# Optimization experiments

Measured on AMD Instinct MI355X. Metric: run time of the kernel, lower is better.

Reference implementation:

```python
import jax, jax.numpy as jnp
import numpy as np

DECAY = 0.99
EPS = 1e-05
N_EMBED = 4096

def setup_inputs() -> dict:
    key = jax.random.key(0)
    k1, k2 = jax.random.split(key)
    x = jax.random.normal(k1, (32, 1024, 256), dtype=jnp.float32)
    embed = jax.random.normal(k2, (256, N_EMBED), dtype=jnp.float32)
    cluster_size = jnp.zeros((N_EMBED,), dtype=jnp.float32)
    embed_avg = embed  # buffer initialized as embed.clone()
    return {"x": x, "embed": embed, "cluster_size": cluster_size, "embed_avg": embed_avg}

def reference(x, embed, cluster_size, embed_avg):
    # x: [B, L, D]; embed/embed_avg: [D, K]; cluster_size: [K]
    B, L, D = x.shape
    K = embed.shape[1]
    flat = x.reshape(B * L, D)
    dist = (jnp.sum(flat * flat, axis=1, keepdims=True)
            - 2.0 * flat @ embed
            + jnp.sum(embed * embed, axis=0, keepdims=True))
    embed_indices = jnp.argmin(dist, axis=1)  # [N]
    # one-hot scatter-sum (counts per code)
    embed_onehot_sum = jnp.zeros((K,), dtype=x.dtype).at[embed_indices].add(1.0)
    # EMA updates, faithful to the torch source including its quirks:
    #   cluster_size.mul_(decay).add_(onehot_sum, alpha=1-eps)  (note: 1-eps, not 1-decay)
    #   embed_avg.mul_(decay).add(embed_sum, ...)  -> .add (not in-place), so embed_sum is discarded
    cluster_size_new = cluster_size * DECAY + embed_onehot_sum * (1.0 - EPS)
    embed_avg_new = embed_avg * DECAY
    n = jnp.sum(cluster_size_new)
    cs = (cluster_size_new + EPS) / (n + K * EPS) * n  # Laplace-smoothed counts
    embed_new = embed_avg_new / cs[None, :]  # [D, K], copied into self.embed before lookup
    # codebook lookup with the UPDATED embed (matches embed.data.copy_ ordering)
    quantize = embed_new.T[embed_indices].reshape(B, L, D)
    diff = jnp.mean(jnp.square(jax.lax.stop_gradient(quantize) - x))
    quantize_st = x + jax.lax.stop_gradient(quantize - x)  # straight-through
    return (quantize_st, embed_indices.reshape(B, L), diff,
            cluster_size_new, embed_avg_new, embed_new)
```

## Files before the change

kernel.cpp:

```cpp
#include <hip/hip_runtime.h>
#include <math.h>

constexpr float DECAY = 0.99f;
constexpr float EPS_F = 1e-5f;
constexpr float MARGIN = 0.08f;

typedef short bf16x8 __attribute__((ext_vector_type(8)));
typedef float f32x4 __attribute__((ext_vector_type(4)));
typedef float vf4 __attribute__((ext_vector_type(4)));

#define BM 256
#define KSPLIT 2
#define NU 128
#define NBUF 6
#define D_FIX 256

__device__ __forceinline__ unsigned rne_bf16(float f) {
  unsigned u = __float_as_uint(f);
  return (u + 0x7fffu + ((u >> 16) & 1u)) >> 16;
}
__device__ __forceinline__ unsigned pack_hilo(float v) {
  unsigned u = __float_as_uint(v);
  unsigned hi = u & 0xffff0000u;
  float rem = v - __uint_as_float(hi);
  return hi | rne_bf16(rem);
}

__global__ void k_prepack_enorm(const float* __restrict__ e, ushort* __restrict__ phl,
                                double* __restrict__ e2d, float* __restrict__ e2f, int K) {
  __shared__ ushort tile[8192];
  __shared__ double red[4][64];
  const int ct = blockIdx.x;
  const int t = threadIdx.x;
  for (int du = 0; du < 4; ++du) {
    __syncthreads();
#pragma unroll
    for (int p = 0; p < 16; ++p) {
      int idx = t + p * 256;
      int dl = idx >> 6, col = idx & 63;
      float v = e[(size_t)(du * 64 + dl) * K + ct * 64 + col];
      unsigned pk = pack_hilo(v);
      int pos = col * 64 + (((dl >> 3) ^ (col & 7)) << 3) + (dl & 7);
      tile[pos] = (ushort)(pk >> 16);
      tile[4096 + pos] = (ushort)(pk & 0xffffu);
    }
    __syncthreads();
    uint4* dst = (uint4*)(phl + (size_t)(ct * 4 + du) * 8192);
    const uint4* srcT = (const uint4*)tile;
#pragma unroll
    for (int p = 0; p < 4; ++p) dst[t + p * 256] = srcT[t + p * 256];
  }
  const int kl = t & 63;
  const int part = t >> 6;
  const int k = ct * 64 + kl;
  double s = 0.0;
  for (int d = part; d < D_FIX; d += 4) {
    double v = (double)e[(size_t)d * K + k];
    s = fma(v, v, s);
  }
  red[part][kl] = s;
  __syncthreads();
  if (part == 0) {
    double tt = ((red[0][kl] + red[1][kl]) + red[2][kl]) + red[3][kl];
    e2d[k] = tt;
    e2f[k] = (float)tt;
  }
}

__launch_bounds__(512, 2)
__global__ void k_argmin_mfma(const float* __restrict__ x, const ushort* __restrict__ phl,
                              const float* __restrict__ e2f,
                              float* __restrict__ bestv, float* __restrict__ secv,
                              int* __restrict__ besti, int N, int K) {
  __shared__ ushort es[NBUF][8192];
  __shared__ float e2s[2048];

  const int tid = threadIdx.x;
  const int l   = tid & 63;
  const int w   = tid >> 6;
  const int g   = l >> 4;
  const int c16 = l & 15;

  const int bflat = blockIdx.x + gridDim.x * blockIdx.y;
  const int xcd   = bflat & 7;
  const int slot  = bflat >> 3;
  const int ytile = xcd >> 2;
  const int xtile = (xcd & 3) * (gridDim.x >> 2) + slot;

  const int kbase = ytile * (K / KSPLIT);
  const int rowW  = xtile * BM + w * 32;

  char* esb = (char*)es;
  const size_t unit0 = (size_t)ytile * NU;

  auto stage = [&](int u) {
    const char* gs = (const char*)phl + ((unit0 + (size_t)u) << 14) + (w << 11) + (l << 4);
    char* ld = esb + ((u % NBUF) << 14) + (w << 11) + (l << 4);
    __builtin_amdgcn_global_load_lds((const unsigned*)gs,          (unsigned*)ld,          16, 0, 0);
    __builtin_amdgcn_global_load_lds((const unsigned*)(gs + 1024), (unsigned*)(ld + 1024), 16, 0, 0);
  };

  for (int i = tid; i < 2048; i += 512) e2s[i] = e2f[kbase + i];

  bf16x8 xh[2][8], xl[2][8];
#pragma unroll
  for (int m = 0; m < 2; ++m) {
    const float* xr = x + (size_t)(rowW + m * 16 + c16) * D_FIX + 8 * g;
#pragma unroll
    for (int t = 0; t < 8; ++t) {
      vf4 fa = __builtin_nontemporal_load((const vf4*)(xr + t * 32));
      vf4 fb = __builtin_nontemporal_load((const vf4*)(xr + t * 32 + 4));
      float f[8] = {fa.x, fa.y, fa.z, fa.w, fb.x, fb.y, fb.z, fb.w};
      union { unsigned u[4]; bf16x8 v; } H, L;
#pragma unroll
      for (int p = 0; p < 4; ++p) {
        unsigned w0 = pack_hilo(f[2 * p]);
        unsigned w1 = pack_hilo(f[2 * p + 1]);
        H.u[p] = (w0 >> 16) | (w1 & 0xffff0000u);
        L.u[p] = (w0 & 0xffffu) | (w1 << 16);
      }
      xh[m][t] = H.v;
      xl[m][t] = L.v;
    }
  }

  float best[2][4], sec[2][4];
  int bidx[2][4];
#pragma unroll
  for (int m = 0; m < 2; ++m)
#pragma unroll
    for (int r = 0; r < 4; ++r) { best[m][r] = 3e38f; sec[m][r] = 3e38f; bidx[m][r] = 0; }

  const int sw16 = ((g ^ (c16 & 7)) << 4);
  const int c16x128 = c16 * 128;

  f32x4 acc[2][4];

  auto compute = [&](int u) {
    const int kt = u >> 2, du = u & 3;
    if (du == 0) {
#pragma unroll
      for (int m = 0; m < 2; ++m)
#pragma unroll
        for (int c = 0; c < 4; ++c) acc[m][c] = (f32x4){0.f, 0.f, 0.f, 0.f};
    }
    const char* pbuf = esb + ((u % NBUF) << 14) + c16x128;
#pragma unroll
    for (int tt = 0; tt < 2; ++tt) {
      const int t = 2 * du + tt;
      const char* pt = pbuf + (sw16 ^ (tt << 6));
#pragma unroll
      for (int c = 0; c < 4; ++c) {
        bf16x8 bh = *(const bf16x8*)(pt + c * 2048);
        bf16x8 bl = *(const bf16x8*)(pt + c * 2048 + 8192);
#pragma unroll
        for (int m = 0; m < 2; ++m) {
          acc[m][c] = __builtin_amdgcn_mfma_f32_16x16x32_bf16(xh[m][t], bh, acc[m][c], 0, 0, 0);
          acc[m][c] = __builtin_amdgcn_mfma_f32_16x16x32_bf16(xh[m][t], bl, acc[m][c], 0, 0, 0);
          acc[m][c] = __builtin_amdgcn_mfma_f32_16x16x32_bf16(xl[m][t], bh, acc[m][c], 0, 0, 0);
        }
      }
    }
    if (du == 3) {
#pragma unroll
      for (int c = 0; c < 4; ++c) {
        const int klocal = kt * 64 + c * 16 + c16;
        const float e2v = e2s[klocal];
        const int kg = kbase + klocal;
#pragma unroll
        for (int m = 0; m < 2; ++m)
#pragma unroll
          for (int r = 0; r < 4; ++r) {
            float dist = fmaf(-2.f, acc[m][c][r], e2v);
            if (dist < best[m][r]) { sec[m][r] = best[m][r]; best[m][r] = dist; bidx[m][r] = kg; }
            else sec[m][r] = fminf(sec[m][r], dist);
          }
      }
    }
  };

  __syncthreads();
  stage(0); stage(1); stage(2); stage(3); stage(4);

  for (int u = 0; u < NU - 5; ++u) {
    asm volatile("s_waitcnt vmcnt(8)" ::: "memory");
    __builtin_amdgcn_s_barrier();
    stage(u + 5);
    compute(u);
  }
  asm volatile("s_waitcnt vmcnt(8)" ::: "memory");
  __builtin_amdgcn_s_barrier();
  compute(NU - 5);
  asm volatile("s_waitcnt vmcnt(6)" ::: "memory");
  __builtin_amdgcn_s_barrier();
  compute(NU - 4);
  asm volatile("s_waitcnt vmcnt(4)" ::: "memory");
  __builtin_amdgcn_s_barrier();
  compute(NU - 3);
  asm volatile("s_waitcnt vmcnt(2)" ::: "memory");
  __builtin_amdgcn_s_barrier();
  compute(NU - 2);
  asm volatile("s_waitcnt vmcnt(0)" ::: "memory");
  __builtin_amdgcn_s_barrier();
  compute(NU - 1);

#pragma unroll
  for (int off = 1; off < 16; off <<= 1) {
#pragma unroll
    for (int m = 0; m < 2; ++m)
#pragma unroll
      for (int r = 0; r < 4; ++r) {
        float ob = __shfl_xor(best[m][r], off);
        float os = __shfl_xor(sec[m][r], off);
        int   oi = __shfl_xor(bidx[m][r], off);
        if (ob < best[m][r] || (ob == best[m][r] && oi < bidx[m][r])) {
          sec[m][r] = fminf(best[m][r], os); best[m][r] = ob; bidx[m][r] = oi;
        } else {
          sec[m][r] = fminf(sec[m][r], ob);
        }
      }
  }

  if (c16 == 0) {
    const size_t base = (size_t)ytile * N;
#pragma unroll
    for (int m = 0; m < 2; ++m)
#pragma unroll
      for (int r = 0; r < 4; ++r) {
        int row = rowW + m * 16 + 4 * g + r;
        bestv[base + row] = best[m][r];
        secv[base + row]  = sec[m][r];
        besti[base + row] = bidx[m][r];
      }
  }
}

__global__ void k_combine(const float* __restrict__ bestv, const float* __restrict__ secv,
                          const int* __restrict__ besti, int* __restrict__ idx_out,
                          float* __restrict__ idxf_out, unsigned int* __restrict__ cnt,
                          int* __restrict__ list, unsigned int* __restrict__ count, int N) {
  int n = blockIdx.x * blockDim.x + threadIdx.x;
  if (n >= N) return;
  float b = bestv[n], s = secv[n];
  int bi = besti[n];
#pragma unroll
  for (int p = 1; p < KSPLIT; ++p) {
    float ob = bestv[(size_t)p * N + n];
    float os = secv[(size_t)p * N + n];
    int   oi = besti[(size_t)p * N + n];
    if (ob < b || (ob == b && oi < bi)) { s = fminf(b, os); b = ob; bi = oi; }
    else s = fminf(s, ob);
  }
  idx_out[n] = bi;
  idxf_out[n] = (float)bi;
  if (s - b < MARGIN) {
    unsigned int p = atomicAdd(count, 1u);
    list[p] = n;
  } else {
    atomicAdd(&cnt[bi], 1u);
  }
}

__launch_bounds__(256, 4)
__global__ void k_rescan(const float* __restrict__ x, const float* __restrict__ e,
                         const double* __restrict__ e2d, const int* __restrict__ list,
                         const unsigned int* __restrict__ count, int* __restrict__ idx_out,
                         float* __restrict__ idxf_out, unsigned int* __restrict__ cnt,
                         int K) {
  __shared__ double xrow[D_FIX];
  __shared__ double rv[256];
  __shared__ int ri[256];
  const int tid = threadIdx.x;
  const unsigned int cntN = *count;
  for (unsigned int ii = blockIdx.x; ii < cntN; ii += gridDim.x) {
    const int row = list[ii];
    __syncthreads();
    xrow[tid] = (double)x[(size_t)row * D_FIX + tid];
    __syncthreads();
    double bb = 1e300; int bi = 0;
    for (int j = 0; j < K; j += 256) {
      const int k = j + tid;
      const float* ek = e + k;
      double a0 = 0.0, a1 = 0.0, a2 = 0.0, a3 = 0.0;
#pragma unroll 8
      for (int d = 0; d < D_FIX; d += 4) {
        a0 = fma(xrow[d + 0], (double)ek[(size_t)(d + 0) * K], a0);
        a1 = fma(xrow[d + 1], (double)ek[(size_t)(d + 1) * K], a1);
        a2 = fma(xrow[d + 2], (double)ek[(size_t)(d + 2) * K], a2);
        a3 = fma(xrow[d + 3], (double)ek[(size_t)(d + 3) * K], a3);
      }
      double dist = e2d[k] - 2.0 * ((a0 + a1) + (a2 + a3));
      if (dist < bb || (dist == bb && k < bi)) { bb = dist; bi = k; }
    }
    rv[tid] = bb; ri[tid] = bi;
    __syncthreads();
    for (int off = 128; off > 0; off >>= 1) {
      if (tid < off) {
        if (rv[tid + off] < rv[tid] || (rv[tid + off] == rv[tid] && ri[tid + off] < ri[tid])) {
          rv[tid] = rv[tid + off]; ri[tid] = ri[tid + off];
        }
      }
      __syncthreads();
    }
    if (tid == 0) {
      idx_out[row] = ri[0];
      idxf_out[row] = (float)ri[0];
      atomicAdd(&cnt[ri[0]], 1u);
    }
    __syncthreads();
  }
}

__global__ void k_cluster(const float* __restrict__ cs_in,
                          const unsigned int* __restrict__ cnt,
                          float* __restrict__ out_csn, float* __restrict__ cs_ws,
                          int K) {
  __shared__ double red[256];
  const int tid = threadIdx.x;
  double s = 0.0;
  for (int k = tid; k < K; k += 256) {
    float csn = cs_in[k] * DECAY + (float)cnt[k] * (1.0f - EPS_F);
    out_csn[k] = csn;
    s += (double)csn;
  }
  red[tid] = s;
  __syncthreads();
  for (int off = 128; off > 0; off >>= 1) {
    if (tid < off) red[tid] += red[tid + off];
    __syncthreads();
  }
  const float n = (float)red[0];
  const float denom = n + (float)K * EPS_F;
  for (int k = tid; k < K; k += 256) {
    float csn = out_csn[k];
    cs_ws[k] = (csn + EPS_F) / denom * n;
  }
}

__global__ void k_embed2(const float* __restrict__ avg_in, const float* __restrict__ cs_ws,
                         float* __restrict__ out_avg, float* __restrict__ out_emb,
                         float* __restrict__ embT, int D, int K) {
  __shared__ float tr[64][65];
  const int kb = blockIdx.x * 64;
  const int db = blockIdx.y * 64;
  const int c = threadIdx.x & 63;
  const int r0 = (threadIdx.x >> 6) * 16;
  const float csv = cs_ws[kb + c];
  for (int i = 0; i < 16; ++i) {
    size_t off = (size_t)(db + r0 + i) * K + kb + c;
    float a = avg_in[off] * DECAY;
    out_avg[off] = a;
    float emb = a / csv;
    out_emb[off] = emb;
    tr[r0 + i][c] = emb;
  }
  __syncthreads();
  for (int i = 0; i < 16; ++i)
    embT[(size_t)(kb + r0 + i) * D + db + c] = tr[c][r0 + i];
}

__global__ void k_gather(const float* __restrict__ x, const float* __restrict__ embT,
                         const int* __restrict__ idx, float* __restrict__ out_q,
                         float* __restrict__ partial) {
  __shared__ float red[256];
  const int tid = threadIdx.x;
  const int n0 = blockIdx.x * 64;
  float s = 0.f;
  for (int u = 0; u < 16; ++u) {
    int i = u * 256 + tid;
    int row = n0 + (i >> 6);
    int f4 = (i & 63) * 4;
    int code = idx[row];
    float4 q  = *(const float4*)&embT[(size_t)code * D_FIX + f4];
    float4 xv = *(const float4*)&x[(size_t)row * D_FIX + f4];
    float4 dv = {q.x - xv.x, q.y - xv.y, q.z - xv.z, q.w - xv.w};
    float4 val = {xv.x + dv.x, xv.y + dv.y, xv.z + dv.z, xv.w + dv.w};
    *(float4*)&out_q[(size_t)row * D_FIX + f4] = val;
    s += dv.x * dv.x + dv.y * dv.y + dv.z * dv.z + dv.w * dv.w;
  }
  red[tid] = s;
  __syncthreads();
  for (int off = 128; off > 0; off >>= 1) {
    if (tid < off) red[tid] += red[tid + off];
    __syncthreads();
  }
  if (tid == 0) partial[blockIdx.x] = red[0];
}

__global__ void k_diff(const float* __restrict__ partial, float* __restrict__ out_diff,
                       int NB, long long total) {
  __shared__ double red[256];
  const int tid = threadIdx.x;
  double s = 0.0;
  for (int i = tid; i < NB; i += 256) s += (double)partial[i];
  red[tid] = s;
  __syncthreads();
  for (int off = 128; off > 0; off >>= 1) {
    if (tid < off) red[tid] += red[tid + off];
    __syncthreads();
  }
  if (tid == 0) out_diff[0] = (float)(red[0] / (double)total);
}

extern "C" void kernel_launch(void* const* d_in, const int* in_sizes, int n_in,
                              void* d_out, int out_size, void* d_ws, size_t ws_size,
                              hipStream_t stream) {
  const float* x            = (const float*)d_in[0];
  const float* embed        = (const float*)d_in[1];
  const float* cluster_size = (const float*)d_in[2];
  const float* embed_avg    = (const float*)d_in[3];

  const int K = in_sizes[2];
  const int D = in_sizes[1] / K;
  const int N = in_sizes[0] / D;

  float* out      = (float*)d_out;
  float* out_q    = out;
  float* out_idx  = out_q + (size_t)N * D;
  float* out_diff = out_idx + N;
  float* out_csn  = out_diff + 1;
  float* out_avg  = out_csn + K;
  float* out_emb  = out_avg + (size_t)D * K;

  ushort* phl = (ushort*)out_avg;

  char* ws = (char*)d_ws;
  double*       e2d     = (double*)ws;               ws += (size_t)K * 8;
  float*        e2f     = (float*)ws;                ws += (size_t)K * 4;
  int*          idx     = (int*)ws;                  ws += (size_t)N * 4;
  unsigned int* cnt     = (unsigned int*)ws;         ws += (size_t)K * 4;
  float*        cs_ws   = (float*)ws;                ws += (size_t)K * 4;
  float*        partial = (float*)ws;                ws += (size_t)(N / 64) * 4;
  float*        bestv   = (float*)ws;                ws += (size_t)KSPLIT * N * 4;
  float*        secv    = (float*)ws;                ws += (size_t)KSPLIT * N * 4;
  int*          besti   = (int*)ws;                  ws += (size_t)KSPLIT * N * 4;
  int*          list    = (int*)ws;                  ws += (size_t)N * 4;
  unsigned int* count   = (unsigned int*)ws;         ws += 64;
  float*        embT    = (float*)ws;                ws += (size_t)K * D * 4;

  hipMemsetAsync(cnt, 0, (size_t)K * sizeof(unsigned int), stream);
  hipMemsetAsync(count, 0, sizeof(unsigned int), stream);

  k_prepack_enorm<<<dim3(K / 64), dim3(256), 0, stream>>>(embed, phl, e2d, e2f, K);
  k_argmin_mfma<<<dim3(N / BM, KSPLIT), dim3(512), 0, stream>>>(x, phl, e2f, bestv, secv,
                                                                besti, N, K);
  k_combine<<<dim3((N + 255) / 256), dim3(256), 0, stream>>>(bestv, secv, besti, idx,
                                                             out_idx, cnt, list, count, N);
  k_rescan<<<dim3(1024), dim3(256), 0, stream>>>(x, embed, e2d, list, count, idx,
                                                 out_idx, cnt, K);
  k_cluster<<<dim3(1), dim3(256), 0, stream>>>(cluster_size, cnt, out_csn, cs_ws, K);
  k_embed2<<<dim3(K / 64, D / 64), dim3(256), 0, stream>>>(embed_avg, cs_ws, out_avg,
                                                           out_emb, embT, D, K);
  k_gather<<<dim3(N / 64), dim3(256), 0, stream>>>(x, embT, idx, out_q, partial);
  k_diff<<<dim3(1), dim3(256), 0, stream>>>(partial, out_diff, N / 64, (long long)N * D);
}
```

Measured before the change: 512.9 us.

## Make argmin kernel codebook-stationary with 128-code LDS slices and streamed rows

Reworks the distance/argmin kernel so each block packs a 128-code slice of the codebook into LDS as hi/lo bf16 once, then loops over 4096 rows of x. This replaces the pipelined async codebook streaming and the separate prepack kernel with a single in-kernel pack. The combine kernel now merges 32 partial results per row instead of 2. In exchange, x is re-read and re-split into hi/lo for every code group, x loads are no longer overlapped with compute, and the 128 KB of LDS per block limits occupancy.

```diff
diff --git a/kernel.cpp b/kernel.cpp
--- a/kernel.cpp
+++ b/kernel.cpp
@@ -9,10 +9,10 @@
 typedef float f32x4 __attribute__((ext_vector_type(4)));
 typedef float vf4 __attribute__((ext_vector_type(4)));
 
-#define BM 256
-#define KSPLIT 2
-#define NU 128
-#define NBUF 6
+#define CB 128
+#define KG 32
+#define RG 8
+#define RB 4096
 #define D_FIX 256
 
 __device__ __forceinline__ unsigned rne_bf16(float f) {
@@ -26,54 +26,33 @@
   return hi | rne_bf16(rem);
 }
 
-__global__ void k_prepack_enorm(const float* __restrict__ e, ushort* __restrict__ phl,
-                                double* __restrict__ e2d, float* __restrict__ e2f, int K) {
-  __shared__ ushort tile[8192];
+__global__ void k_enorm(const float* __restrict__ e, double* __restrict__ e2d,
+                        float* __restrict__ e2f, int D, int K) {
   __shared__ double red[4][64];
-  const int ct = blockIdx.x;
-  const int t = threadIdx.x;
-  for (int du = 0; du < 4; ++du) {
-    __syncthreads();
-#pragma unroll
-    for (int p = 0; p < 16; ++p) {
-      int idx = t + p * 256;
-      int dl = idx >> 6, col = idx & 63;
-      float v = e[(size_t)(du * 64 + dl) * K + ct * 64 + col];
-      unsigned pk = pack_hilo(v);
-      int pos = col * 64 + (((dl >> 3) ^ (col & 7)) << 3) + (dl & 7);
-      tile[pos] = (ushort)(pk >> 16);
-      tile[4096 + pos] = (ushort)(pk & 0xffffu);
-    }
-    __syncthreads();
-    uint4* dst = (uint4*)(phl + (size_t)(ct * 4 + du) * 8192);
-    const uint4* srcT = (const uint4*)tile;
-#pragma unroll
-    for (int p = 0; p < 4; ++p) dst[t + p * 256] = srcT[t + p * 256];
-  }
-  const int kl = t & 63;
-  const int part = t >> 6;
-  const int k = ct * 64 + kl;
+  const int kl = threadIdx.x & 63;
+  const int part = threadIdx.x >> 6;
+  const int k = blockIdx.x * 64 + kl;
   double s = 0.0;
-  for (int d = part; d < D_FIX; d += 4) {
+  for (int d = part; d < D; d += 4) {
     double v = (double)e[(size_t)d * K + k];
     s = fma(v, v, s);
   }
   red[part][kl] = s;
   __syncthreads();
   if (part == 0) {
-    double tt = ((red[0][kl] + red[1][kl]) + red[2][kl]) + red[3][kl];
-    e2d[k] = tt;
-    e2f[k] = (float)tt;
+    double t = ((red[0][kl] + red[1][kl]) + red[2][kl]) + red[3][kl];
+    e2d[k] = t;
+    e2f[k] = (float)t;
   }
 }
 
 __launch_bounds__(512, 2)
-__global__ void k_argmin_mfma(const float* __restrict__ x, const ushort* __restrict__ phl,
+__global__ void k_argmin_mfma(const float* __restrict__ x, const float* __restrict__ e,
                               const float* __restrict__ e2f,
                               float* __restrict__ bestv, float* __restrict__ secv,
                               int* __restrict__ besti, int N, int K) {
-  __shared__ ushort es[NBUF][8192];
-  __shared__ float e2s[2048];
+  __shared__ ushort esE[8 * 8192];
+  __shared__ float e2s[CB];
 
   const int tid = threadIdx.x;
   const int l   = tid & 63;
@@ -81,157 +60,132 @@
   const int g   = l >> 4;
   const int c16 = l & 15;
 
-  const int bflat = blockIdx.x + gridDim.x * blockIdx.y;
-  const int xcd   = bflat & 7;
-  const int slot  = bflat >> 3;
-  const int ytile = xcd >> 2;
-  const int xtile = (xcd & 3) * (gridDim.x >> 2) + slot;
-
-  const int kbase = ytile * (K / KSPLIT);
-  const int rowW  = xtile * BM + w * 32;
-
-  char* esb = (char*)es;
-  const size_t unit0 = (size_t)ytile * NU;
-
-  auto stage = [&](int u) {
-    const char* gs = (const char*)phl + ((unit0 + (size_t)u) << 14) + (w << 11) + (l << 4);
-    char* ld = esb + ((u % NBUF) << 14) + (w << 11) + (l << 4);
-    __builtin_amdgcn_global_load_lds((const unsigned*)gs,          (unsigned*)ld,          16, 0, 0);
-    __builtin_amdgcn_global_load_lds((const unsigned*)(gs + 1024), (unsigned*)(ld + 1024), 16, 0, 0);
-  };
-
-  for (int i = tid; i < 2048; i += 512) e2s[i] = e2f[kbase + i];
-
-  bf16x8 xh[2][8], xl[2][8];
-#pragma unroll
-  for (int m = 0; m < 2; ++m) {
-    const float* xr = x + (size_t)(rowW + m * 16 + c16) * D_FIX + 8 * g;
-#pragma unroll
-    for (int t = 0; t < 8; ++t) {
-      vf4 fa = __builtin_nontemporal_load((const vf4*)(xr + t * 32));
-      vf4 fb = __builtin_nontemporal_load((const vf4*)(xr + t * 32 + 4));
-      float f[8] = {fa.x, fa.y, fa.z, fa.w, fb.x, fb.y, fb.z, fb.w};
-      union { unsigned u[4]; bf16x8 v; } H, L;
-#pragma unroll
-      for (int p = 0; p < 4; ++p) {
-        unsigned w0 = pack_hilo(f[2 * p]);
-        unsigned w1 = pack_hilo(f[2 * p + 1]);
-        H.u[p] = (w0 >> 16) | (w1 & 0xffff0000u);
-        L.u[p] = (w0 & 0xffffu) | (w1 << 16);
+  const int rg = blockIdx.x;
+  const int kg = blockIdx.y;
+  const int kbase = kg * CB;
+  const int rowbase = rg * RB + w * 512;
+
+  char* esb = (char*)esE;
+
+  for (int i = tid; i < CB * D_FIX; i += 512) {
+    const int col = i & (CB - 1);
+    const int d   = i >> 7;
+    float v = e[(size_t)d * K + kbase + col];
+    unsigned pk = pack_hilo(v);
+    const int cb = col >> 6, du = d >> 6;
+    const int col_l = col & 63, dl = d & 63;
+    const int pos = col_l * 64 + (((dl >> 3) ^ (col_l & 7)) << 3) + (dl & 7);
+    const int ub = (cb * 4 + du) * 8192;
+    esE[ub + pos] = (ushort)(pk >> 16);
+    esE[ub + 4096 + pos] = (ushort)(pk & 0xffffu);
+  }
+  if (tid < CB) e2s[tid] = e2f[kbase + tid];
+  __syncthreads();
+
+  const int sw16 = ((g ^ (c16 & 7)) << 4);
+  const size_t kgN = (size_t)kg * N;
+
+  for (int rt = 0; rt < 16; ++rt) {
+    const int row0 = rowbase + rt * 32;
+
+    bf16x8 xh[2][8], xl[2][8];
+#pragma unroll
+    for (int m = 0; m < 2; ++m) {
+      const float* xr = x + (size_t)(row0 + m * 16 + c16) * D_FIX + 8 * g;
+#pragma unroll
+      for (int t = 0; t < 8; ++t) {
+        vf4 fa = *(const vf4*)(xr + t * 32);
+        vf4 fb = *(const vf4*)(xr + t * 32 + 4);
+        float f[8] = {fa.x, fa.y, fa.z, fa.w, fb.x, fb.y, fb.z, fb.w};
+        union { unsigned u[4]; bf16x8 v; } H, L;
+#pragma unroll
+        for (int p = 0; p < 4; ++p) {
+          unsigned w0 = pack_hilo(f[2 * p]);
+          unsigned w1 = pack_hilo(f[2 * p + 1]);
+          H.u[p] = (w0 >> 16) | (w1 & 0xffff0000u);
+          L.u[p] = (w0 & 0xffffu) | (w1 << 16);
+        }
+        xh[m][t] = H.v;
+        xl[m][t] = L.v;
       }
-      xh[m][t] = H.v;
-      xl[m][t] = L.v;
-    }
-  }
-
-  float best[2][4], sec[2][4];
-  int bidx[2][4];
-#pragma unroll
-  for (int m = 0; m < 2; ++m)
-#pragma unroll
-    for (int r = 0; r < 4; ++r) { best[m][r] = 3e38f; sec[m][r] = 3e38f; bidx[m][r] = 0; }
-
-  const int sw16 = ((g ^ (c16 & 7)) << 4);
-  const int c16x128 = c16 * 128;
-
-  f32x4 acc[2][4];
-
-  auto compute = [&](int u) {
-    const int kt = u >> 2, du = u & 3;
-    if (du == 0) {
+    }
+
+    f32x4 acc[2][8];
+#pragma unroll
+    for (int m = 0; m < 2; ++m)
+#pragma unroll
+      for (int c = 0; c < 8; ++c) acc[m][c] = (f32x4){0.f, 0.f, 0.f, 0.f};
+
+#pragma unroll
+    for (int du = 0; du < 4; ++du) {
+#pragma unroll
+      for (int tt = 0; tt < 2; ++tt) {
+        const int t = du * 2 + tt;
+#pragma unroll
+        for (int c = 0; c < 8; ++c) {
+          const char* pt = esb + (((c >> 2) * 4 + du) << 14) + ((c & 3) * 2048)
+                         + c16 * 128 + (sw16 ^ (tt << 6));
+          bf16x8 bh = *(const bf16x8*)pt;
+          bf16x8 bl = *(const bf16x8*)(pt + 8192);
+#pragma unroll
+          for (int m = 0; m < 2; ++m) {
+            acc[m][c] = __builtin_amdgcn_mfma_f32_16x16x32_bf16(xh[m][t], bh, acc[m][c], 0, 0, 0);
+            acc[m][c] = __builtin_amdgcn_mfma_f32_16x16x32_bf16(xh[m][t], bl, acc[m][c], 0, 0, 0);
+            acc[m][c] = __builtin_amdgcn_mfma_f32_16x16x32_bf16(xl[m][t], bh, acc[m][c], 0, 0, 0);
+          }
+        }
+      }
+    }
+
+    float best[2][4], sec[2][4];
+    int bidx[2][4];
+#pragma unroll
+    for (int m = 0; m < 2; ++m)
+#pragma unroll
+      for (int r = 0; r < 4; ++r) { best[m][r] = 3e38f; sec[m][r] = 3e38f; bidx[m][r] = 0; }
+
+#pragma unroll
+    for (int c = 0; c < 8; ++c) {
+      const float e2v = e2s[c * 16 + c16];
+      const int kgk = kbase + c * 16 + c16;
 #pragma unroll
       for (int m = 0; m < 2; ++m)
 #pragma unroll
-        for (int c = 0; c < 4; ++c) acc[m][c] = (f32x4){0.f, 0.f, 0.f, 0.f};
-    }
-    const char* pbuf = esb + ((u % NBUF) << 14) + c16x128;
-#pragma unroll
-    for (int tt = 0; tt < 2; ++tt) {
-      const int t = 2 * du + tt;
-      const char* pt = pbuf + (sw16 ^ (tt << 6));
-#pragma unroll
-      for (int c = 0; c < 4; ++c) {
-        bf16x8 bh = *(const bf16x8*)(pt + c * 2048);
-        bf16x8 bl = *(const bf16x8*)(pt + c * 2048 + 8192);
-#pragma unroll
-        for (int m = 0; m < 2; ++m) {
-          acc[m][c] = __builtin_amdgcn_mfma_f32_16x16x32_bf16(xh[m][t], bh, acc[m][c], 0, 0, 0);
-          acc[m][c] = __builtin_amdgcn_mfma_f32_16x16x32_bf16(xh[m][t], bl, acc[m][c], 0, 0, 0);
-          acc[m][c] = __builtin_amdgcn_mfma_f32_16x16x32_bf16(xl[m][t], bh, acc[m][c], 0, 0, 0);
-        }
-      }
-    }
-    if (du == 3) {
-#pragma unroll
-      for (int c = 0; c < 4; ++c) {
-        const int klocal = kt * 64 + c * 16 + c16;
-        const float e2v = e2s[klocal];
-        const int kg = kbase + klocal;
-#pragma unroll
-        for (int m = 0; m < 2; ++m)
-#pragma unroll
-          for (int r = 0; r < 4; ++r) {
-            float dist = fmaf(-2.f, acc[m][c][r], e2v);
-            if (dist < best[m][r]) { sec[m][r] = best[m][r]; best[m][r] = dist; bidx[m][r] = kg; }
-            else sec[m][r] = fminf(sec[m][r], dist);
+        for (int r = 0; r < 4; ++r) {
+          float dist = fmaf(-2.f, acc[m][c][r], e2v);
+          if (dist < best[m][r]) { sec[m][r] = best[m][r]; best[m][r] = dist; bidx[m][r] = kgk; }
+          else sec[m][r] = fminf(sec[m][r], dist);
+        }
+    }
+
+#pragma unroll
+    for (int off = 1; off < 16; off <<= 1) {
+#pragma unroll
+      for (int m = 0; m < 2; ++m)
+#pragma unroll
+        for (int r = 0; r < 4; ++r) {
+          float ob = __shfl_xor(best[m][r], off);
+          float os = __shfl_xor(sec[m][r], off);
+          int   oi = __shfl_xor(bidx[m][r], off);
+          if (ob < best[m][r] || (ob == best[m][r] && oi < bidx[m][r])) {
+            sec[m][r] = fminf(best[m][r], os); best[m][r] = ob; bidx[m][r] = oi;
+          } else {
+            sec[m][r] = fminf(sec[m][r], ob);
           }
-      }
-    }
-  };
-
-  __syncthreads();
-  stage(0); stage(1); stage(2); stage(3); stage(4);
-
-  for (int u = 0; u < NU - 5; ++u) {
-    asm volatile("s_waitcnt vmcnt(8)" ::: "memory");
-    __builtin_amdgcn_s_barrier();
-    stage(u + 5);
-    compute(u);
-  }
-  asm volatile("s_waitcnt vmcnt(8)" ::: "memory");
-  __builtin_amdgcn_s_barrier();
-  compute(NU - 5);
-  asm volatile("s_waitcnt vmcnt(6)" ::: "memory");
-  __builtin_amdgcn_s_barrier();
-  compute(NU - 4);
-  asm volatile("s_waitcnt vmcnt(4)" ::: "memory");
-  __builtin_amdgcn_s_barrier();
-  compute(NU - 3);
-  asm volatile("s_waitcnt vmcnt(2)" ::: "memory");
-  __builtin_amdgcn_s_barrier();
-  compute(NU - 2);
-  asm volatile("s_waitcnt vmcnt(0)" ::: "memory");
-  __builtin_amdgcn_s_barrier();
-  compute(NU - 1);
-
-#pragma unroll
-  for (int off = 1; off < 16; off <<= 1) {
-#pragma unroll
-    for (int m = 0; m < 2; ++m)
-#pragma unroll
-      for (int r = 0; r < 4; ++r) {
-        float ob = __shfl_xor(best[m][r], off);
-        float os = __shfl_xor(sec[m][r], off);
-        int   oi = __shfl_xor(bidx[m][r], off);
-        if (ob < best[m][r] || (ob == best[m][r] && oi < bidx[m][r])) {
-          sec[m][r] = fminf(best[m][r], os); best[m][r] = ob; bidx[m][r] = oi;
-        } else {
-          sec[m][r] = fminf(sec[m][r], ob);
-        }
-      }
-  }
-
-  if (c16 == 0) {
-    const size_t base = (size_t)ytile * N;
-#pragma unroll
-    for (int m = 0; m < 2; ++m)
-#pragma unroll
-      for (int r = 0; r < 4; ++r) {
-        int row = rowW + m * 16 + 4 * g + r;
-        bestv[base + row] = best[m][r];
-        secv[base + row]  = sec[m][r];
-        besti[base + row] = bidx[m][r];
-      }
+        }
+    }
+
+    if (c16 == 0) {
+#pragma unroll
+      for (int m = 0; m < 2; ++m)
+#pragma unroll
+        for (int r = 0; r < 4; ++r) {
+          int row = row0 + m * 16 + 4 * g + r;
+          bestv[kgN + row] = best[m][r];
+          secv[kgN + row]  = sec[m][r];
+          besti[kgN + row] = bidx[m][r];
+        }
+    }
   }
 }
 
@@ -243,8 +197,8 @@
   if (n >= N) return;
   float b = bestv[n], s = secv[n];
   int bi = besti[n];
-#pragma unroll
-  for (int p = 1; p < KSPLIT; ++p) {
+#pragma unroll 4
+  for (int p = 1; p < KG; ++p) {
     float ob = bestv[(size_t)p * N + n];
     float os = secv[(size_t)p * N + n];
     int   oi = besti[(size_t)p * N + n];
@@ -422,8 +376,6 @@
   float* out_avg  = out_csn + K;
   float* out_emb  = out_avg + (size_t)D * K;
 
-  ushort* phl = (ushort*)out_avg;
-
   char* ws = (char*)d_ws;
   double*       e2d     = (double*)ws;               ws += (size_t)K * 8;
   float*        e2f     = (float*)ws;                ws += (size_t)K * 4;
@@ -431,9 +383,9 @@
   unsigned int* cnt     = (unsigned int*)ws;         ws += (size_t)K * 4;
   float*        cs_ws   = (float*)ws;                ws += (size_t)K * 4;
   float*        partial = (float*)ws;                ws += (size_t)(N / 64) * 4;
-  float*        bestv   = (float*)ws;                ws += (size_t)KSPLIT * N * 4;
-  float*        secv    = (float*)ws;                ws += (size_t)KSPLIT * N * 4;
-  int*          besti   = (int*)ws;                  ws += (size_t)KSPLIT * N * 4;
+  float*        bestv   = (float*)ws;                ws += (size_t)KG * N * 4;
+  float*        secv    = (float*)ws;                ws += (size_t)KG * N * 4;
+  int*          besti   = (int*)ws;                  ws += (size_t)KG * N * 4;
   int*          list    = (int*)ws;                  ws += (size_t)N * 4;
   unsigned int* count   = (unsigned int*)ws;         ws += 64;
   float*        embT    = (float*)ws;                ws += (size_t)K * D * 4;
@@ -441,9 +393,9 @@
   hipMemsetAsync(cnt, 0, (size_t)K * sizeof(unsigned int), stream);
   hipMemsetAsync(count, 0, sizeof(unsigned int), stream);
 
-  k_prepack_enorm<<<dim3(K / 64), dim3(256), 0, stream>>>(embed, phl, e2d, e2f, K);
-  k_argmin_mfma<<<dim3(N / BM, KSPLIT), dim3(512), 0, stream>>>(x, phl, e2f, bestv, secv,
-                                                                besti, N, K);
+  k_enorm<<<dim3(K / 64), dim3(256), 0, stream>>>(embed, e2d, e2f, D, K);
+  k_argmin_mfma<<<dim3(RG, KG), dim3(512), 0, stream>>>(x, embed, e2f, bestv, secv,
+                                                        besti, N, K);
   k_combine<<<dim3((N + 255) / 256), dim3(256), 0, stream>>>(bestv, secv, besti, idx,
                                                              out_idx, cnt, list, count, N);
   k_rescan<<<dim3(1024), dim3(256), 0, stream>>>(x, embed, e2d, list, count, idx,
```

Result: slower. 938.1 us (+82.9%).
